# Kernel optimization log

Measured on AMD Instinct MI355X. Metric: run time of the kernel, lower is better.

Reference implementation:

```python
import jax, jax.numpy as jnp
import numpy as np

EPS = 1e-6  # flax nn.LayerNorm default epsilon


def excl_cumsum(a, axis):
    c = jnp.roll(jnp.cumsum(a, axis=axis), 1, axis=axis)
    idx = [slice(None)] * a.ndim
    idx[axis] = slice(0, 1)
    return c.at[tuple(idx)].set(0.0)


def mixed_chunk_attn(q, k, v, n_chunks):
    # Mixed chunk linear attention (https://arxiv.org/pdf/2202.10447.pdf)
    if n_chunks == 1:
        mask = jnp.tri(q.shape[1], q.shape[1], -1, dtype=q.dtype)
        qk = jnp.einsum('bls,bms->blm', q, k) * mask
        return jnp.einsum('blm,bme->ble', qk, v)
    B, L = q.shape[:2]
    C = L // n_chunks
    qc = q.reshape(B, n_chunks, C, -1)
    kc = k.reshape(B, n_chunks, C, -1)
    vc = v.reshape(B, n_chunks, C, -1)
    # global linear attention across chunks (exclusive prefix of kv states)
    kv = excl_cumsum(jnp.einsum('bgcs,bgce->bgse', kc, vc), axis=1)
    glob = jnp.einsum('bgcs,bgse->bgce', qc, kv)
    # local strictly-causal quadratic attention within each chunk
    mask = jnp.tri(C, C, -1, dtype=q.dtype)
    qk = jnp.einsum('bgns,bgms->bgnm', qc, kc) * mask
    loc = jnp.einsum('bgnm,bgme->bgne', qk, vc)
    return (glob + loc).reshape(B, L, -1)


def ln_normalize(x):
    mu = jnp.mean(x, axis=-1, keepdims=True)
    var = jnp.mean(jnp.square(x - mu), axis=-1, keepdims=True)
    return (x - mu) * jax.lax.rsqrt(var + EPS)


def fwblock(x, labels, weights, W1, b1, W2, b2, ln_scale, ln_bias, Wu, bu, step_sizes, n_chunks):
    B, L, D = x.shape
    F = W1.shape[1]

    # slow-weight forward with zero perturbations; grad wrt perturbations gives
    # per-token gradients at each layer's output (rank-one fast-weight updates).
    def slow_loss(p1, p3, p_scale, p_bias):
        h1 = x @ W1 + b1 + p1                    # FWDense(4D) + output perturbation
        h2 = jnp.square(jax.nn.relu(h1))         # FWSquaredRelu (paramless)
        h3 = h2 @ W2 + b2 + p3                   # FWDense(D) + output perturbation
        h4 = ln_normalize(h3) * (ln_scale + p_scale) + (ln_bias + p_bias)
        logits = h4 @ Wu + bu
        ll = -jnp.sum(jax.nn.log_softmax(logits) * labels, axis=-1)
        loss = jnp.sum(weights * ll) / jnp.maximum(jnp.sum(weights), 1e-8)
        return loss, h2

    zeros = (jnp.zeros((B, L, F), x.dtype), jnp.zeros((B, L, D), x.dtype),
             jnp.zeros((B, L, D), x.dtype), jnp.zeros((B, L, D), x.dtype))
    (g1, g3, g_scale, g_bias), h2_slow = jax.grad(
        slow_loss, argnums=(0, 1, 2, 3), has_aux=True)(*zeros)

    # fast-weight forward: rank-one weight updates expressed as causal linear attn
    x1 = x @ W1 + b1 - step_sizes[0] * mixed_chunk_attn(x, x, g1, n_chunks)
    x2 = jnp.square(jax.nn.relu(x1))             # step_sizes[1] unused (no params)
    x3 = x2 @ W2 + b2 - step_sizes[2] * mixed_chunk_attn(x2, h2_slow, g3, n_chunks)
    fast_scale = ln_scale - step_sizes[3] * excl_cumsum(g_scale, axis=1)
    fast_bias = ln_bias - step_sizes[3] * excl_cumsum(g_bias, axis=1)
    x4 = ln_normalize(x3) * fast_scale + fast_bias
    return x4 @ Wu + bu


def setup_inputs():
    key = jax.random.key(0)
    ks = jax.random.split(key, 6)
    B, L, D, V = 2, 2048, 1024, 8192
    F = 4 * D
    x = jax.random.normal(ks[0], (B, L, D), jnp.float32)
    labels = jax.random.uniform(ks[1], (B, L, V), jnp.float32)
    weights = jnp.ones((B, L), jnp.float32)
    W1 = jax.random.normal(ks[2], (D, F), jnp.float32) / np.sqrt(D).astype(np.float32)
    b1 = jnp.zeros((F,), jnp.float32)
    W2 = jax.random.normal(ks[3], (F, D), jnp.float32) / np.sqrt(F).astype(np.float32)
    b2 = jnp.zeros((D,), jnp.float32)
    ln_scale = jnp.ones((D,), jnp.float32)
    ln_bias = jnp.zeros((D,), jnp.float32)
    Wu = jax.random.normal(ks[4], (D, V), jnp.float32) / np.sqrt(D).astype(np.float32)
    bu = jnp.zeros((V,), jnp.float32)
    step_sizes = jnp.full((4,), 0.01, jnp.float32)
    return dict(x=x, labels=labels, weights=weights, W1=W1, b1=b1, W2=W2, b2=b2,
                ln_scale=ln_scale, ln_bias=ln_bias, Wu=Wu, bu=bu,
                step_sizes=step_sizes, n_chunks=16)


def reference(x, labels, weights, W1, b1, W2, b2, ln_scale, ln_bias, Wu, bu, step_sizes, n_chunks):
    return fwblock(x, labels, weights, W1, b1, W2, b2, ln_scale, ln_bias, Wu, bu, step_sizes, n_chunks)
```

## Files before the change

kernel.cpp:

```cpp
#include <hip/hip_runtime.h>
#include <cstdint>

typedef unsigned short ushort_t;
typedef __bf16 bf16x8 __attribute__((ext_vector_type(8)));
typedef float f32x4 __attribute__((ext_vector_type(4)));
typedef ushort_t us8 __attribute__((ext_vector_type(8)));

__device__ __forceinline__ ushort_t f2bf(float f) {
  union { float f; unsigned int u; } v; v.f = f;
  unsigned int u = v.u;
  unsigned int r = (u + 0x7fffu + ((u >> 16) & 1u)) >> 16;
  return (ushort_t)r;
}
__device__ __forceinline__ float bf2f(ushort_t u) {
  union { unsigned int u; float f; } v; v.u = ((unsigned int)u) << 16; return v.f;
}

#define GLOAD16(gp, lp)                                                              \
  __builtin_amdgcn_global_load_lds(                                                  \
      reinterpret_cast<const __attribute__((address_space(1))) unsigned int*>(       \
          reinterpret_cast<uintptr_t>(gp)),                                          \
      reinterpret_cast<__attribute__((address_space(3))) unsigned int*>(             \
          reinterpret_cast<uintptr_t>(lp)),                                          \
      16, 0, 0)

struct GemmP {
  const ushort_t* A; const ushort_t* B;
  int M, N, K;
  long long sA, sB;
  float* outf;   long long sOutF;
  ushort_t* outb; long long sOutB;
  ushort_t* outb2;
  const float* bias;
  const float* auxf; long long sAuxF;
  const ushort_t* auxb;
  const float* steps;
  float* part; int ksplit, Kc, Tt;
};

template <int EPI>
__global__ __launch_bounds__(256) void gemm_bt(GemmP p) {
  const int nwg = gridDim.x * gridDim.y;
  const int orig = blockIdx.y * gridDim.x + blockIdx.x;
  const int xcd = orig & 7, loc = orig >> 3;
  const int q8 = nwg >> 3, r8 = nwg & 7;
  const int wg = (xcd < r8) ? (xcd * (q8 + 1) + loc) : (r8 * (q8 + 1) + (xcd - r8) * q8 + loc);
  int mt, nt;
  if (EPI == 7) {
    int t_ = wg;
    mt = (int)((sqrtf(8.f * t_ + 1.f) - 1.f) * 0.5f);
    while ((mt + 1) * (mt + 2) / 2 <= t_) mt++;
    while (mt * (mt + 1) / 2 > t_) mt--;
    nt = t_ - mt * (mt + 1) / 2;
  } else {
    nt = wg % gridDim.x; mt = wg / gridDim.x;
  }
  const int m0 = mt * 128, n0 = nt * 128;

  int bz = blockIdx.z, ks = 0;
  if (EPI == 6 || EPI == 7) { bz = blockIdx.z / p.ksplit; ks = blockIdx.z % p.ksplit; }

  const ushort_t* A = p.A + (size_t)bz * p.sA;
  const ushort_t* B = p.B + (size_t)bz * p.sB;

  int kbeg = 0, kend = p.K;
  if (EPI == 6 || EPI == 7) { kbeg = ks * p.Kc; kend = kbeg + p.Kc; }
  else if (EPI == 4 || EPI == 5) kend = min(p.K, m0 + 128);

  __shared__ ushort_t sA[2 * 128 * 32];
  __shared__ ushort_t sB[2 * 128 * 32];

  const int tid = threadIdx.x;
  const int wid = tid >> 6, lane = tid & 63;
  const int wm = wid >> 1, wn = wid & 1;

  f32x4 acc[4][4];
#pragma unroll
  for (int i = 0; i < 4; i++)
#pragma unroll
    for (int j = 0; j < 4; j++) acc[i][j] = f32x4{0.f, 0.f, 0.f, 0.f};

  const int lr = lane >> 2;
  const int lcsw = (((lane & 3) ^ ((lr >> 1) & 3)) * 8);
  const int rA0 = wid * 16 + lr;
  const int rA1 = 64 + wid * 16 + lr;
  const ushort_t* gA0 = A + (size_t)(m0 + rA0) * p.K + lcsw;
  const ushort_t* gA1 = A + (size_t)(m0 + rA1) * p.K + lcsw;
  const ushort_t* gB0 = B + (size_t)(n0 + rA0) * p.K + lcsw;
  const ushort_t* gB1 = B + (size_t)(n0 + rA1) * p.K + lcsw;
  ushort_t* lA0 = &sA[wid * 512];
  ushort_t* lA1 = &sA[(4 + wid) * 512];
  ushort_t* lB0 = &sB[wid * 512];
  ushort_t* lB1 = &sB[(4 + wid) * 512];

  const int fr = lane & 15;
  const int q = lane >> 4;
  const int slot = (q ^ ((fr >> 1) & 3)) * 8;
  int offA[4], offB[4];
#pragma unroll
  for (int i = 0; i < 4; i++) offA[i] = (wm * 4 + i) * 512 + fr * 32 + slot;
#pragma unroll
  for (int j = 0; j < 4; j++) offB[j] = (wn * 4 + j) * 512 + fr * 32 + slot;

  const int nT = (kend - kbeg) >> 5;
  auto stage = [&](int t) {
    const int kk = kbeg + t * 32;
    const int o = (t & 1) * 4096;
    GLOAD16(gA0 + kk, lA0 + o);
    GLOAD16(gA1 + kk, lA1 + o);
    GLOAD16(gB0 + kk, lB0 + o);
    GLOAD16(gB1 + kk, lB1 + o);
  };
  stage(0);
  asm volatile("s_waitcnt vmcnt(0)" ::: "memory");
  __builtin_amdgcn_s_barrier();

  for (int t = 0; t < nT; ++t) {
    const int co = (t & 1) * 4096;
    if (t + 1 < nT) stage(t + 1);
    __builtin_amdgcn_sched_barrier(0);
    bf16x8 av[4], bv[4];
#pragma unroll
    for (int j = 0; j < 4; j++) bv[j] = *reinterpret_cast<const bf16x8*>(&sB[co + offB[j]]);
#pragma unroll
    for (int i = 0; i < 4; i++) av[i] = *reinterpret_cast<const bf16x8*>(&sA[co + offA[i]]);
    __builtin_amdgcn_s_setprio(1);
#pragma unroll
    for (int i = 0; i < 4; i++)
#pragma unroll
      for (int j = 0; j < 4; j++)
        acc[i][j] = __builtin_amdgcn_mfma_f32_16x16x32_bf16(av[i], bv[j], acc[i][j], 0, 0, 0);
    __builtin_amdgcn_s_setprio(0);
    asm volatile("s_waitcnt vmcnt(0)" ::: "memory");
    __builtin_amdgcn_s_barrier();
  }

  const int fq = q;
  float ss = 0.f;
  if (EPI == 4) ss = p.steps[0];
  else if (EPI == 5) ss = p.steps[2];
  float* outf = p.outf ? p.outf + (size_t)bz * p.sOutF : nullptr;
  ushort_t* outb = p.outb ? p.outb + (size_t)bz * p.sOutB : nullptr;
  ushort_t* outb2 = p.outb2;
  const float* auxf = p.auxf ? p.auxf + (size_t)bz * p.sAuxF : nullptr;
  const ushort_t* auxb = p.auxb ? p.auxb + (size_t)bz * p.sAuxF : nullptr;
  float* partT = nullptr;
  if (EPI == 6) partT = p.part + (size_t)blockIdx.z * p.M * p.N;
  if (EPI == 7) partT = p.part + ((size_t)blockIdx.z * p.Tt + wg) * 16384;

#pragma unroll
  for (int i = 0; i < 4; i++) {
#pragma unroll
    for (int j = 0; j < 4; j++) {
#pragma unroll
      for (int r2 = 0; r2 < 4; r2++) {
        int lrow = wm * 64 + i * 16 + fq * 4 + r2;
        int lcol = wn * 64 + j * 16 + fr;
        int row = m0 + lrow, col = n0 + lcol;
        size_t g = (size_t)row * p.N + col;
        float v = acc[i][j][r2];
        if (EPI == 0) {
          outf[g] = v + (p.bias ? p.bias[col] : 0.f);
        } else if (EPI == 8) {
          outb[g] = f2bf(v + p.bias[col]);
        } else if (EPI == 1) {
          v += p.bias[col];
          outb[g] = f2bf(v);
          float rl = fmaxf(v, 0.f);
          outb2[g] = f2bf(rl * rl);
        } else if (EPI == 2) {
          outb[g] = f2bf(v * 2.f * sqrtf(bf2f(auxb[g])));
        } else if (EPI == 4) {
          float x1 = bf2f(auxb[g]) - ss * v;
          float rl = fmaxf(x1, 0.f);
          outb[g] = f2bf(rl * rl);
        } else if (EPI == 5) {
          outf[g] = auxf[g] - ss * v;
        } else if (EPI == 6) {
          partT[g] = v;
        } else if (EPI == 7) {
          partT[lrow * 128 + lcol] = v;
        }
      }
    }
  }
}

template <int EPI>
__global__ __launch_bounds__(512, 2) void gemm256(GemmP p) {
  const int nwg = gridDim.x * gridDim.y;
  const int orig = blockIdx.y * gridDim.x + blockIdx.x;
  const int xcd = orig & 7, loc = orig >> 3;
  const int q8 = nwg >> 3, r8 = nwg & 7;
  const int wg = (xcd < r8) ? (xcd * (q8 + 1) + loc) : (r8 * (q8 + 1) + (xcd - r8) * q8 + loc);
  const int nt = wg % gridDim.x, mt = wg / gridDim.x;
  const int m0 = mt * 256, n0 = nt * 256;
  const int bz = blockIdx.z;

  const ushort_t* A = p.A + (size_t)bz * p.sA;
  const ushort_t* B = p.B + (size_t)bz * p.sB;
  const int kend = p.K;

  extern __shared__ ushort_t smem[];
  ushort_t* sA = smem;
  ushort_t* sB = smem + 4 * 8192;

  const int tid = threadIdx.x;
  const int wid = tid >> 6, lane = tid & 63;
  const int wm = wid >> 2, wn = wid & 3;

  f32x4 acc[8][4];
#pragma unroll
  for (int i = 0; i < 8; i++)
#pragma unroll
    for (int j = 0; j < 4; j++) acc[i][j] = f32x4{0.f, 0.f, 0.f, 0.f};

  const int lr = lane >> 2;
  const int lcsw = (((lane & 3) ^ ((lr >> 1) & 3)) * 8);
  const int rT0 = wid * 16 + lr;
  const int rT1 = 128 + wid * 16 + lr;
  const ushort_t* gA0 = A + (size_t)(m0 + rT0) * p.K + lcsw;
  const ushort_t* gA1 = A + (size_t)(m0 + rT1) * p.K + lcsw;
  const ushort_t* gB0 = B + (size_t)(n0 + rT0) * p.K + lcsw;
  const ushort_t* gB1 = B + (size_t)(n0 + rT1) * p.K + lcsw;
  ushort_t* lA0 = &sA[wid * 512];
  ushort_t* lA1 = &sA[(8 + wid) * 512];
  ushort_t* lB0 = &sB[wid * 512];
  ushort_t* lB1 = &sB[(8 + wid) * 512];

  const int fr = lane & 15;
  const int q = lane >> 4;
  const int slot = (q ^ ((fr >> 1) & 3)) * 8;
  int offA[8], offB[4];
#pragma unroll
  for (int i = 0; i < 8; i++) offA[i] = (wm * 8 + i) * 512 + fr * 32 + slot;
#pragma unroll
  for (int j = 0; j < 4; j++) offB[j] = (wn * 4 + j) * 512 + fr * 32 + slot;

  const int nT = kend >> 5;
  auto stage4 = [&](int t) {
    const int kk = t * 32;
    const int o = (t & 3) * 8192;
    GLOAD16(gA0 + kk, lA0 + o);
    GLOAD16(gA1 + kk, lA1 + o);
    GLOAD16(gB0 + kk, lB0 + o);
    GLOAD16(gB1 + kk, lB1 + o);
  };
  stage4(0);
  if (nT > 1) stage4(1);
  if (nT > 2) stage4(2);
  if (nT > 2)      { asm volatile("s_waitcnt vmcnt(8)" ::: "memory"); }
  else if (nT > 1) { asm volatile("s_waitcnt vmcnt(4)" ::: "memory"); }
  else             { asm volatile("s_waitcnt vmcnt(0)" ::: "memory"); }
  __builtin_amdgcn_s_barrier();

  for (int t = 0; t < nT; ++t) {
    const int co = (t & 3) * 8192;
    if (t + 3 < nT) stage4(t + 3);
    __builtin_amdgcn_sched_barrier(0);
    bf16x8 av[8], bv[4];
#pragma unroll
    for (int j = 0; j < 4; j++) bv[j] = *reinterpret_cast<const bf16x8*>(&sB[co + offB[j]]);
#pragma unroll
    for (int i = 0; i < 8; i++) av[i] = *reinterpret_cast<const bf16x8*>(&sA[co + offA[i]]);
    __builtin_amdgcn_s_setprio(1);
#pragma unroll
    for (int i = 0; i < 8; i++)
#pragma unroll
      for (int j = 0; j < 4; j++)
        acc[i][j] = __builtin_amdgcn_mfma_f32_16x16x32_bf16(av[i], bv[j], acc[i][j], 0, 0, 0);
    __builtin_amdgcn_s_setprio(0);
    if (t + 3 < nT)      { asm volatile("s_waitcnt vmcnt(8)" ::: "memory"); }
    else if (t + 2 < nT) { asm volatile("s_waitcnt vmcnt(4)" ::: "memory"); }
    else if (t + 1 < nT) { asm volatile("s_waitcnt vmcnt(0)" ::: "memory"); }
    __builtin_amdgcn_s_barrier();
  }

  const int fq = q;
  float* outf = p.outf;
  ushort_t* outb = p.outb;

#pragma unroll
  for (int i = 0; i < 8; i++) {
#pragma unroll
    for (int j = 0; j < 4; j++) {
#pragma unroll
      for (int r2 = 0; r2 < 4; r2++) {
        int row = m0 + wm * 128 + i * 16 + fq * 4 + r2;
        int col = n0 + wn * 64 + j * 16 + fr;
        size_t g = (size_t)row * p.N + col;
        float v = acc[i][j][r2];
        if (EPI == 0) {
          outf[g] = v + p.bias[col];
        } else if (EPI == 8) {
          outb[g] = f2bf(v + p.bias[col]);
        }
      }
    }
  }
}

__global__ __launch_bounds__(256) void k_comb(const float* part, const float* bias, float* out,
                                              int N, size_t MN, int S) {
  size_t e = ((size_t)blockIdx.x * 256 + threadIdx.x) * 4;
  if (e >= MN) return;
  float4 s = *(const float4*)(part + e);
  for (int p_ = 1; p_ < S; p_++) {
    float4 v = *(const float4*)(part + (size_t)p_ * MN + e);
    s.x += v.x; s.y += v.y; s.z += v.z; s.w += v.w;
  }
  if (bias) {
    int col = (int)(e % (size_t)N);
    s.x += bias[col]; s.y += bias[col + 1]; s.z += bias[col + 2]; s.w += bias[col + 3];
  }
  *(float4*)(out + e) = s;
}

__global__ __launch_bounds__(256) void k_combtri(const float* part, ushort_t* out, int Tt, int S,
                                                 int L) {
  int t = blockIdx.x, bz = blockIdx.y;
  int mt = (int)((sqrtf(8.f * t + 1.f) - 1.f) * 0.5f);
  while ((mt + 1) * (mt + 2) / 2 <= t) mt++;
  while (mt * (mt + 1) / 2 > t) mt--;
  int nt = t - mt * (mt + 1) / 2;
  const float* pb = part + ((size_t)bz * S * Tt + t) * 16384;
  ushort_t* ob = out + (size_t)bz * L * L;
  for (int e4 = threadIdx.x; e4 < 4096; e4 += 256) {
    int e = e4 * 4;
    float4 s = *(const float4*)(pb + e);
    for (int p_ = 1; p_ < S; p_++) {
      float4 v = *(const float4*)(pb + (size_t)p_ * Tt * 16384 + e);
      s.x += v.x; s.y += v.y; s.z += v.z; s.w += v.w;
    }
    int lr = e >> 7, lc2 = e & 127;
    int row = mt * 128 + lr, col = nt * 128 + lc2;
    ushort4 o;
    o.x = (col < row) ? f2bf(s.x) : (ushort_t)0;
    o.y = (col + 1 < row) ? f2bf(s.y) : (ushort_t)0;
    o.z = (col + 2 < row) ? f2bf(s.z) : (ushort_t)0;
    o.w = (col + 3 < row) ? f2bf(s.w) : (ushort_t)0;
    *(ushort4*)(&ob[(size_t)row * L + col]) = o;
  }
}

__global__ __launch_bounds__(256) void k_conv(const float* in, ushort_t* out, size_t n) {
  size_t i = ((size_t)blockIdx.x * 256 + threadIdx.x) * 4;
  if (i >= n) return;
  float4 v = *(const float4*)(in + i);
  out[i] = f2bf(v.x); out[i + 1] = f2bf(v.y); out[i + 2] = f2bf(v.z); out[i + 3] = f2bf(v.w);
}

__global__ __launch_bounds__(256) void k_tconv(const float* in, ushort_t* out, int R, int C) {
  __shared__ float t[32][33];
  int c0 = blockIdx.x * 32, r0 = blockIdx.y * 32;
  int tx = threadIdx.x & 31, ty = threadIdx.x >> 5;
#pragma unroll
  for (int i = ty; i < 32; i += 8) t[i][tx] = in[(size_t)(r0 + i) * C + c0 + tx];
  __syncthreads();
#pragma unroll
  for (int i = ty; i < 32; i += 8) out[(size_t)(c0 + i) * R + r0 + tx] = f2bf(t[tx][i]);
}

__global__ __launch_bounds__(256) void k_wprep(const float* in, ushort_t* outS, ushort_t* outT,
                                               int R, int C) {
  __shared__ float t[32][33];
  int c0 = blockIdx.x * 32, r0 = blockIdx.y * 32;
  int tx = threadIdx.x & 31, ty = threadIdx.x >> 5;
#pragma unroll
  for (int i = ty; i < 32; i += 8) {
    float v = in[(size_t)(r0 + i) * C + c0 + tx];
    t[i][tx] = v;
    outS[(size_t)(r0 + i) * C + c0 + tx] = f2bf(v);
  }
  __syncthreads();
#pragma unroll
  for (int i = ty; i < 32; i += 8) outT[(size_t)(c0 + i) * R + r0 + tx] = f2bf(t[tx][i]);
}

__global__ __launch_bounds__(256) void k_tb2b(const ushort_t* in, ushort_t* out, int L, int C) {
  __shared__ ushort_t t[32][33];
  int b = blockIdx.z;
  const ushort_t* ib = in + (size_t)b * L * C;
  ushort_t* ob = out + (size_t)b * C * L;
  int c0 = blockIdx.x * 32, l0 = blockIdx.y * 32;
  int tx = threadIdx.x & 31, ty = threadIdx.x >> 5;
#pragma unroll
  for (int i = ty; i < 32; i += 8) t[i][tx] = ib[(size_t)(l0 + i) * C + c0 + tx];
  __syncthreads();
#pragma unroll
  for (int i = ty; i < 32; i += 8) ob[(size_t)(c0 + i) * L + l0 + tx] = t[tx][i];
}

__device__ __forceinline__ void blockRed2(float& a, float& b, float* red) {
#pragma unroll
  for (int o = 32; o; o >>= 1) { a += __shfl_down(a, o); b += __shfl_down(b, o); }
  int w = threadIdx.x >> 6;
  if ((threadIdx.x & 63) == 0) { red[w] = a; red[4 + w] = b; }
  __syncthreads();
  a = red[0] + red[1] + red[2] + red[3];
  b = red[4] + red[5] + red[6] + red[7];
  __syncthreads();
}

__global__ __launch_bounds__(256) void k_lncomb(const float* part, const float* bias,
                                                const float* sc, const float* bi, float* nout,
                                                float* rstd, ushort_t* yb, size_t MN, int D,
                                                int S) {
  __shared__ float red[8];
  int row = blockIdx.x;
  int d = threadIdx.x * 4;
  size_t g = (size_t)row * D + d;
  float4 v = *(const float4*)(part + g);
  for (int s_ = 1; s_ < S; s_++) {
    float4 w = *(const float4*)(part + (size_t)s_ * MN + g);
    v.x += w.x; v.y += w.y; v.z += w.z; v.w += w.w;
  }
  float4 bb = *(const float4*)(bias + d);
  v.x += bb.x; v.y += bb.y; v.z += bb.z; v.w += bb.w;
  float s1 = v.x + v.y + v.z + v.w;
  float s2 = v.x * v.x + v.y * v.y + v.z * v.z + v.w * v.w;
  blockRed2(s1, s2, red);
  float mu = s1 / D;
  float var = s2 / D - mu * mu;
  float rs = rsqrtf(var + 1e-6f);
  float4 nv;
  nv.x = (v.x - mu) * rs; nv.y = (v.y - mu) * rs; nv.z = (v.z - mu) * rs; nv.w = (v.w - mu) * rs;
  *(float4*)(nout + g) = nv;
  float4 scv = *(const float4*)(sc + d);
  float4 biv = *(const float4*)(bi + d);
  ushort4 o;
  o.x = f2bf(nv.x * scv.x + biv.x);
  o.y = f2bf(nv.y * scv.y + biv.y);
  o.z = f2bf(nv.z * scv.z + biv.z);
  o.w = f2bf(nv.w * scv.w + biv.w);
  *(ushort4*)(yb + g) = o;
  if (threadIdx.x == 0) rstd[row] = rs;
}

__global__ __launch_bounds__(256) void k_lnfwd2(const float* X, const float* fs, const float* fb,
                                                ushort_t* yb, int D) {
  __shared__ float red[8];
  int row = blockIdx.x;
  const float* x = X + (size_t)row * D;
  float s = 0.f, s2 = 0.f;
  for (int d = threadIdx.x; d < D; d += 256) { float v = x[d]; s += v; s2 += v * v; }
  blockRed2(s, s2, red);
  float mu = s / D;
  float var = s2 / D - mu * mu;
  float rs = rsqrtf(var + 1e-6f);
  for (int d = threadIdx.x; d < D; d += 256) {
    size_t g = (size_t)row * D + d;
    float nv = (x[d] - mu) * rs;
    yb[g] = f2bf(nv * fs[g] + fb[g]);
  }
}

__global__ __launch_bounds__(256) void k_lnbwd(const float* G, const float* nn, const float* rstd,
                                               const float* sc, ushort_t* g3b, float* gsc, int D) {
  __shared__ float red[8];
  int row = blockIdx.x;
  const float* g = G + (size_t)row * D;
  const float* n_ = nn + (size_t)row * D;
  float sa = 0.f, sb = 0.f;
  for (int d = threadIdx.x; d < D; d += 256) {
    float dn = g[d] * sc[d];
    sa += dn; sb += dn * n_[d];
  }
  blockRed2(sa, sb, red);
  float a = sa / D, b = sb / D, rs = rstd[row];
  for (int d = threadIdx.x; d < D; d += 256) {
    size_t gi = (size_t)row * D + d;
    float dn = g[d] * sc[d];
    g3b[gi] = f2bf(rs * (dn - a - n_[d] * b));
    gsc[gi] = g[d] * n_[d];
  }
}

__global__ __launch_bounds__(256) void k_wsum(const float* w, float* o, int n) {
  __shared__ float red[4];
  float s = 0.f;
  for (int i = threadIdx.x; i < n; i += 256) s += w[i];
#pragma unroll
  for (int d = 32; d; d >>= 1) s += __shfl_down(s, d);
  if ((threadIdx.x & 63) == 0) red[threadIdx.x >> 6] = s;
  __syncthreads();
  if (threadIdx.x == 0) o[0] = fmaxf(red[0] + red[1] + red[2] + red[3], 1e-8f);
}

__global__ __launch_bounds__(256) void k_softgrad(const ushort_t* logits, const float* labels,
                                                  const float* w, const float* wsum,
                                                  ushort_t* dlb, int V) {
  __shared__ float red[8];
  const int row = blockIdx.x;
  const int tid = threadIdx.x;
  const ushort_t* l = logits + (size_t)row * V + tid * 32;
  const float* y = labels + (size_t)row * V + tid * 32;
  float lv[32], yv[32];
#pragma unroll
  for (int i = 0; i < 4; i++) {
    us8 u = *reinterpret_cast<const us8*>(l + i * 8);
#pragma unroll
    for (int j = 0; j < 8; j++) lv[i * 8 + j] = bf2f(u[j]);
  }
#pragma unroll
  for (int i = 0; i < 8; i++) {
    float4 v = *reinterpret_cast<const float4*>(y + i * 4);
    yv[i * 4] = v.x; yv[i * 4 + 1] = v.y; yv[i * 4 + 2] = v.z; yv[i * 4 + 3] = v.w;
  }
  float m = lv[0], t = yv[0];
#pragma unroll
  for (int i = 1; i < 32; i++) { m = fmaxf(m, lv[i]); t += yv[i]; }
#pragma unroll
  for (int o = 32; o; o >>= 1) { m = fmaxf(m, __shfl_down(m, o)); t += __shfl_down(t, o); }
  int wv = tid >> 6;
  if ((tid & 63) == 0) { red[wv] = m; red[4 + wv] = t; }
  __syncthreads();
  m = fmaxf(fmaxf(red[0], red[1]), fmaxf(red[2], red[3]));
  t = red[4] + red[5] + red[6] + red[7];
  __syncthreads();
  float s = 0.f;
#pragma unroll
  for (int i = 0; i < 32; i++) { lv[i] = expf(lv[i] - m); s += lv[i]; }
#pragma unroll
  for (int o = 32; o; o >>= 1) s += __shfl_down(s, o);
  if ((tid & 63) == 0) red[wv] = s;
  __syncthreads();
  s = red[0] + red[1] + red[2] + red[3];
  float c = w[row] / wsum[0];
  float ci = c * t / s;
  ushort_t* dl = dlb + (size_t)row * V + tid * 32;
#pragma unroll
  for (int i = 0; i < 4; i++) {
    us8 o;
#pragma unroll
    for (int j = 0; j < 8; j++) o[j] = f2bf(ci * lv[i * 8 + j] - c * yv[i * 8 + j]);
    *reinterpret_cast<us8*>(dl + i * 8) = o;
  }
}

__global__ __launch_bounds__(256) void k_scanpart(const float* gs, const float* gb, float* ps,
                                                  float* pb, int L, int D) {
  int d = blockIdx.x * 256 + threadIdx.x;
  int seg = blockIdx.y, b = blockIdx.z;
  const int SEGL = L / 16;
  size_t base = ((size_t)b * L + seg * SEGL) * D + d;
  float s1 = 0.f, s2 = 0.f;
  for (int i = 0; i < SEGL; i++) { s1 += gs[base + (size_t)i * D]; s2 += gb[base + (size_t)i * D]; }
  size_t pi = ((size_t)b * 16 + seg) * D + d;
  ps[pi] = s1; pb[pi] = s2;
}

__global__ __launch_bounds__(256) void k_scanapply(const float* gs, const float* gb,
                                                   const float* ps, const float* pb,
                                                   const float* sc, const float* bi,
                                                   const float* steps, float* fs, float* fb,
                                                   int L, int D) {
  int d = blockIdx.x * 256 + threadIdx.x;
  int seg = blockIdx.y, b = blockIdx.z;
  const int SEGL = L / 16;
  float ss = steps[3];
  float rs_ = 0.f, rb_ = 0.f;
  for (int s = 0; s < seg; s++) {
    size_t pi = ((size_t)b * 16 + s) * D + d;
    rs_ += ps[pi]; rb_ += pb[pi];
  }
  float s0 = sc[d], b0 = bi[d];
  size_t base = ((size_t)b * L + seg * SEGL) * D + d;
  for (int i = 0; i < SEGL; i++) {
    size_t g = base + (size_t)i * D;
    fs[g] = s0 - ss * rs_;
    fb[g] = b0 - ss * rb_;
    rs_ += gs[g]; rb_ += gb[g];
  }
}

extern "C" void kernel_launch(void* const* d_in, const int* in_sizes, int n_in, void* d_out,
                              int out_size, void* d_ws, size_t ws_size, hipStream_t stream) {
  const float* x        = (const float*)d_in[0];
  const float* labels   = (const float*)d_in[1];
  const float* weights  = (const float*)d_in[2];
  const float* W1       = (const float*)d_in[3];
  const float* b1       = (const float*)d_in[4];
  const float* W2       = (const float*)d_in[5];
  const float* b2       = (const float*)d_in[6];
  const float* ln_scale = (const float*)d_in[7];
  const float* ln_bias  = (const float*)d_in[8];
  const float* Wu       = (const float*)d_in[9];
  const float* bu       = (const float*)d_in[10];
  const float* steps    = (const float*)d_in[11];

  const int BL = in_sizes[2];
  const int D  = in_sizes[7];
  const int F  = in_sizes[4];
  const int V  = in_sizes[10];
  const int Bb = 2, L = BL / Bb;
  const int T1t = (L / 128) * (L / 128 + 1) / 2;
  const unsigned SMEM = 4 * 8192 * 2 * 2;

  char* ws = (char*)d_ws;
  size_t off = 0;
  auto take = [&](size_t b) { char* p = ws + off; off = (off + b + 255) & ~(size_t)255; return p; };

  ushort_t* xb   = (ushort_t*)take((size_t)BL * D * 2);
  ushort_t* w1t  = (ushort_t*)take((size_t)F * D * 2);
  ushort_t* w2t  = (ushort_t*)take((size_t)D * F * 2);
  ushort_t* w2b  = (ushort_t*)take((size_t)F * D * 2);
  ushort_t* wut  = (ushort_t*)take((size_t)V * D * 2);
  ushort_t* wub  = (ushort_t*)take((size_t)D * V * 2);
  ushort_t* H1b  = (ushort_t*)take((size_t)BL * F * 2);
  ushort_t* H2b  = (ushort_t*)take((size_t)BL * F * 2);
  float*    nbuf = (float*)take((size_t)BL * D * 4);
  float*    rstd = (float*)take((size_t)BL * 4);
  ushort_t* h4b  = (ushort_t*)take((size_t)BL * D * 2);
  float*    wsumb= (float*)take(256);
  float*    G4   = (float*)take((size_t)BL * D * 4);
  float*    gsc  = (float*)take((size_t)BL * D * 4);
  ushort_t* g3b  = (ushort_t*)take((size_t)BL * D * 2);
  ushort_t* g3t  = (ushort_t*)take((size_t)BL * D * 2);
  float*    fs   = (float*)take((size_t)BL * D * 4);
  float*    fb   = (float*)take((size_t)BL * D * 4);
  ushort_t* x4b  = (ushort_t*)take((size_t)BL * D * 2);
  float*    psc  = (float*)take((size_t)Bb * 16 * D * 4);
  float*    pbi  = (float*)take((size_t)Bb * 16 * D * 4);
  char* poolA = take((size_t)BL * V * 4);
  ushort_t* logitsb = (ushort_t*)poolA;
  float*    partA  = (float*)poolA;
  ushort_t* g1b = (ushort_t*)poolA;
  ushort_t* g1t = (ushort_t*)(poolA + (size_t)BL * F * 2);
  ushort_t* S1b = (ushort_t*)(poolA + (size_t)BL * F * 4);
  ushort_t* x2b = (ushort_t*)(poolA + (size_t)BL * F * 4 + (size_t)Bb * L * L * 2);
  char* poolB = take((size_t)BL * V * 2);
  ushort_t* dlb = (ushort_t*)poolB;
  float*    partS1 = (float*)poolB;
  ushort_t* S2b = (ushort_t*)poolB;
  float*    X3  = (float*)(poolB + (size_t)Bb * L * L * 2);
  float*    x3  = (float*)(poolB + (size_t)Bb * L * L * 2 + (size_t)BL * D * 4);

  dim3 blk(256), blk5(512);
  const size_t MN_D = (size_t)BL * D;

  k_conv<<<dim3((unsigned)((size_t)BL * D / 1024)), blk, 0, stream>>>(x, xb, (size_t)BL * D);
  k_tconv<<<dim3(F / 32, D / 32), blk, 0, stream>>>(W1, w1t, D, F);
  k_wprep<<<dim3(D / 32, F / 32), blk, 0, stream>>>(W2, w2b, w2t, F, D);
  k_wprep<<<dim3(V / 32, D / 32), blk, 0, stream>>>(Wu, wub, wut, D, V);

  GemmP p;
  auto clr = [&]() { p = GemmP{}; };

  clr(); p.A = xb; p.B = w1t; p.M = BL; p.N = F; p.K = D;
  p.outb = H1b; p.outb2 = H2b; p.bias = b1;
  gemm_bt<1><<<dim3(F / 128, BL / 128, 1), blk, 0, stream>>>(p);
  clr(); p.A = H2b; p.B = w2t; p.M = BL; p.N = D; p.K = F;
  p.part = partA; p.ksplit = 4; p.Kc = F / 4;
  gemm_bt<6><<<dim3(D / 128, BL / 128, 4), blk, 0, stream>>>(p);
  k_lncomb<<<dim3(BL), blk, 0, stream>>>(partA, b2, ln_scale, ln_bias, nbuf, rstd, h4b, MN_D, D, 4);
  clr(); p.A = h4b; p.B = wut; p.M = BL; p.N = V; p.K = D; p.outb = logitsb; p.bias = bu;
  gemm256<8><<<dim3(V / 256, BL / 256, 1), blk5, SMEM, stream>>>(p);
  k_wsum<<<dim3(1), blk, 0, stream>>>(weights, wsumb, BL);
  k_softgrad<<<dim3(BL), blk, 0, stream>>>(logitsb, labels, weights, wsumb, dlb, V);
  clr(); p.A = dlb; p.B = wub; p.M = BL; p.N = D; p.K = V;
  p.part = partA; p.ksplit = 4; p.Kc = V / 4;
  gemm_bt<6><<<dim3(D / 128, BL / 128, 4), blk, 0, stream>>>(p);
  k_comb<<<dim3((unsigned)(MN_D / 1024)), blk, 0, stream>>>(partA, nullptr, G4, D, MN_D, 4);
  k_lnbwd<<<dim3(BL), blk, 0, stream>>>(G4, nbuf, rstd, ln_scale, g3b, gsc, D);
  clr(); p.A = g3b; p.B = w2b; p.M = BL; p.N = F; p.K = D; p.outb = g1b; p.auxb = H2b;
  gemm_bt<2><<<dim3(F / 128, BL / 128, 1), blk, 0, stream>>>(p);
  k_tb2b<<<dim3(F / 32, L / 32, Bb), blk, 0, stream>>>(g1b, g1t, L, F);
  k_tb2b<<<dim3(D / 32, L / 32, Bb), blk, 0, stream>>>(g3b, g3t, L, D);
  clr(); p.A = xb; p.B = xb; p.M = L; p.N = L; p.K = D;
  p.sA = (long long)L * D; p.sB = (long long)L * D;
  p.part = partS1; p.ksplit = 2; p.Kc = D / 2; p.Tt = T1t;
  gemm_bt<7><<<dim3(T1t, 1, Bb * 2), blk, 0, stream>>>(p);
  k_combtri<<<dim3(T1t, Bb), blk, 0, stream>>>(partS1, S1b, T1t, 2, L);
  clr(); p.A = S1b; p.B = g1t; p.M = L; p.N = F; p.K = L;
  p.sA = (long long)L * L; p.sB = (long long)F * L;
  p.outb = x2b; p.sOutB = (long long)L * F; p.auxb = H1b; p.sAuxF = (long long)L * F;
  p.steps = steps;
  gemm_bt<4><<<dim3(F / 128, L / 128, Bb), blk, 0, stream>>>(p);
  clr(); p.A = x2b; p.B = w2t; p.M = BL; p.N = D; p.K = F;
  p.part = partA; p.ksplit = 4; p.Kc = F / 4;
  gemm_bt<6><<<dim3(D / 128, BL / 128, 4), blk, 0, stream>>>(p);
  k_comb<<<dim3((unsigned)(MN_D / 1024)), blk, 0, stream>>>(partA, b2, X3, D, MN_D, 4);
  clr(); p.A = x2b; p.B = H2b; p.M = L; p.N = L; p.K = F;
  p.sA = (long long)L * F; p.sB = (long long)L * F;
  p.part = partA; p.ksplit = 2; p.Kc = F / 2; p.Tt = T1t;
  gemm_bt<7><<<dim3(T1t, 1, Bb * 2), blk, 0, stream>>>(p);
  k_combtri<<<dim3(T1t, Bb), blk, 0, stream>>>(partA, S2b, T1t, 2, L);
  clr(); p.A = S2b; p.B = g3t; p.M = L; p.N = D; p.K = L;
  p.sA = (long long)L * L; p.sB = (long long)D * L;
  p.outf = x3; p.sOutF = (long long)L * D; p.auxf = X3; p.sAuxF = (long long)L * D; p.steps = steps;
  gemm_bt<5><<<dim3(D / 128, L / 128, Bb), blk, 0, stream>>>(p);
  k_scanpart<<<dim3(D / 256, 16, Bb), blk, 0, stream>>>(gsc, G4, psc, pbi, L, D);
  k_scanapply<<<dim3(D / 256, 16, Bb), blk, 0, stream>>>(gsc, G4, psc, pbi, ln_scale, ln_bias,
                                                         steps, fs, fb, L, D);
  k_lnfwd2<<<dim3(BL), blk, 0, stream>>>(x3, fs, fb, x4b, D);
  clr(); p.A = x4b; p.B = wut; p.M = BL; p.N = V; p.K = D; p.outf = (float*)d_out; p.bias = bu;
  gemm256<0><<<dim3(V / 256, BL / 256, 1), blk5, SMEM, stream>>>(p);
}
```

Measured before the change: 1.103 ms.

## Replace direct global-to-LDS loads with register-staged double-buffered GEMM pipeline

Both GEMM kernels stop using global_load_lds and instead load tiles into registers, then write them to LDS one phase later, with two register sets alternating across an unrolled-by-two loop. The 256-tile kernel drops from a 4-stage LDS ring to 2 stages, which halves shared memory, and its min-blocks launch bound is removed. The intent is to hide global latency behind compute using registers rather than LDS depth. In exchange it costs more VGPRs and adds explicit LDS store instructions, and losing the occupancy hint may reduce occupancy. The gemm256 kernel also drops the blockIdx.z batch offset.

```diff
diff --git a/kernel.cpp b/kernel.cpp
--- a/kernel.cpp
+++ b/kernel.cpp
@@ -5,6 +5,7 @@
 typedef __bf16 bf16x8 __attribute__((ext_vector_type(8)));
 typedef float f32x4 __attribute__((ext_vector_type(4)));
 typedef ushort_t us8 __attribute__((ext_vector_type(8)));
+typedef unsigned int u32x4 __attribute__((ext_vector_type(4)));
 
 __device__ __forceinline__ ushort_t f2bf(float f) {
   union { float f; unsigned int u; } v; v.f = f;
@@ -15,14 +16,6 @@
 __device__ __forceinline__ float bf2f(ushort_t u) {
   union { unsigned int u; float f; } v; v.u = ((unsigned int)u) << 16; return v.f;
 }
-
-#define GLOAD16(gp, lp)                                                              \
-  __builtin_amdgcn_global_load_lds(                                                  \
-      reinterpret_cast<const __attribute__((address_space(1))) unsigned int*>(       \
-          reinterpret_cast<uintptr_t>(gp)),                                          \
-      reinterpret_cast<__attribute__((address_space(3))) unsigned int*>(             \
-          reinterpret_cast<uintptr_t>(lp)),                                          \
-      16, 0, 0)
 
 struct GemmP {
   const ushort_t* A; const ushort_t* B;
@@ -37,6 +30,19 @@
   const float* steps;
   float* part; int ksplit, Kc, Tt;
 };
+
+
+#define LOADT_BT(t, S)                                                        \
+  { const int kk_ = kbeg + (t) * 32;                                          \
+    rA0##S = *(const u32x4*)(gA0 + kk_); rA1##S = *(const u32x4*)(gA1 + kk_); \
+    rB0##S = *(const u32x4*)(gB0 + kk_); rB1##S = *(const u32x4*)(gB1 + kk_); }
+#define STORET_BT(o, S)                                                       \
+  { *(u32x4*)(wA0 + (o)) = rA0##S; *(u32x4*)(wA1 + (o)) = rA1##S;             \
+    *(u32x4*)(wB0 + (o)) = rB0##S; *(u32x4*)(wB1 + (o)) = rB1##S; }
+#define PHASE_END()                                                           \
+  { asm volatile("s_waitcnt lgkmcnt(0)" ::: "memory");                        \
+    __builtin_amdgcn_sched_barrier(0);                                        \
+    __builtin_amdgcn_s_barrier(); }
 
 template <int EPI>
 __global__ __launch_bounds__(256) void gemm_bt(GemmP p) {
@@ -82,16 +88,16 @@
 
   const int lr = lane >> 2;
   const int lcsw = (((lane & 3) ^ ((lr >> 1) & 3)) * 8);
-  const int rA0 = wid * 16 + lr;
-  const int rA1 = 64 + wid * 16 + lr;
-  const ushort_t* gA0 = A + (size_t)(m0 + rA0) * p.K + lcsw;
-  const ushort_t* gA1 = A + (size_t)(m0 + rA1) * p.K + lcsw;
-  const ushort_t* gB0 = B + (size_t)(n0 + rA0) * p.K + lcsw;
-  const ushort_t* gB1 = B + (size_t)(n0 + rA1) * p.K + lcsw;
-  ushort_t* lA0 = &sA[wid * 512];
-  ushort_t* lA1 = &sA[(4 + wid) * 512];
-  ushort_t* lB0 = &sB[wid * 512];
-  ushort_t* lB1 = &sB[(4 + wid) * 512];
+  const int rA0r = wid * 16 + lr;
+  const int rA1r = 64 + wid * 16 + lr;
+  const ushort_t* gA0 = A + (size_t)(m0 + rA0r) * p.K + lcsw;
+  const ushort_t* gA1 = A + (size_t)(m0 + rA1r) * p.K + lcsw;
+  const ushort_t* gB0 = B + (size_t)(n0 + rA0r) * p.K + lcsw;
+  const ushort_t* gB1 = B + (size_t)(n0 + rA1r) * p.K + lcsw;
+  ushort_t* wA0 = &sA[wid * 512 + lane * 8];
+  ushort_t* wA1 = &sA[(4 + wid) * 512 + lane * 8];
+  ushort_t* wB0 = &sB[wid * 512 + lane * 8];
+  ushort_t* wB1 = &sB[(4 + wid) * 512 + lane * 8];
 
   const int fr = lane & 15;
   const int q = lane >> 4;
@@ -103,22 +109,10 @@
   for (int j = 0; j < 4; j++) offB[j] = (wn * 4 + j) * 512 + fr * 32 + slot;
 
   const int nT = (kend - kbeg) >> 5;
-  auto stage = [&](int t) {
-    const int kk = kbeg + t * 32;
-    const int o = (t & 1) * 4096;
-    GLOAD16(gA0 + kk, lA0 + o);
-    GLOAD16(gA1 + kk, lA1 + o);
-    GLOAD16(gB0 + kk, lB0 + o);
-    GLOAD16(gB1 + kk, lB1 + o);
-  };
-  stage(0);
-  asm volatile("s_waitcnt vmcnt(0)" ::: "memory");
-  __builtin_amdgcn_s_barrier();
-
-  for (int t = 0; t < nT; ++t) {
-    const int co = (t & 1) * 4096;
-    if (t + 1 < nT) stage(t + 1);
-    __builtin_amdgcn_sched_barrier(0);
+  u32x4 rA0e, rA1e, rB0e, rB1e;
+  u32x4 rA0o, rA1o, rB0o, rB1o;
+
+  auto compute = [&](int co) {
     bf16x8 av[4], bv[4];
 #pragma unroll
     for (int j = 0; j < 4; j++) bv[j] = *reinterpret_cast<const bf16x8*>(&sB[co + offB[j]]);
@@ -131,8 +125,24 @@
       for (int j = 0; j < 4; j++)
         acc[i][j] = __builtin_amdgcn_mfma_f32_16x16x32_bf16(av[i], bv[j], acc[i][j], 0, 0, 0);
     __builtin_amdgcn_s_setprio(0);
-    asm volatile("s_waitcnt vmcnt(0)" ::: "memory");
-    __builtin_amdgcn_s_barrier();
+  };
+
+  LOADT_BT(0, e);
+  STORET_BT(0, e);
+  if (nT > 1) LOADT_BT(1, o);
+  PHASE_END();
+
+  for (int t = 0; t < nT; t += 2) {
+    compute(0);
+    if (t + 1 < nT) STORET_BT(4096, o);
+    if (t + 2 < nT) LOADT_BT(t + 2, e);
+    PHASE_END();
+    if (t + 1 < nT) {
+      compute(4096);
+      if (t + 2 < nT) STORET_BT(0, e);
+      if (t + 3 < nT) LOADT_BT(t + 3, o);
+      PHASE_END();
+    }
   }
 
   const int fq = q;
@@ -187,7 +197,7 @@
 }
 
 template <int EPI>
-__global__ __launch_bounds__(512, 2) void gemm256(GemmP p) {
+__global__ __launch_bounds__(512) void gemm256(GemmP p) {
   const int nwg = gridDim.x * gridDim.y;
   const int orig = blockIdx.y * gridDim.x + blockIdx.x;
   const int xcd = orig & 7, loc = orig >> 3;
@@ -195,15 +205,14 @@
   const int wg = (xcd < r8) ? (xcd * (q8 + 1) + loc) : (r8 * (q8 + 1) + (xcd - r8) * q8 + loc);
   const int nt = wg % gridDim.x, mt = wg / gridDim.x;
   const int m0 = mt * 256, n0 = nt * 256;
-  const int bz = blockIdx.z;
-
-  const ushort_t* A = p.A + (size_t)bz * p.sA;
-  const ushort_t* B = p.B + (size_t)bz * p.sB;
-  const int kend = p.K;
+
+  const ushort_t* A = p.A;
+  const ushort_t* B = p.B;
+  const int kbeg = 0, kend = p.K;
 
   extern __shared__ ushort_t smem[];
   ushort_t* sA = smem;
-  ushort_t* sB = smem + 4 * 8192;
+  ushort_t* sB = smem + 2 * 8192;
 
   const int tid = threadIdx.x;
   const int wid = tid >> 6, lane = tid & 63;
@@ -223,10 +232,10 @@
   const ushort_t* gA1 = A + (size_t)(m0 + rT1) * p.K + lcsw;
   const ushort_t* gB0 = B + (size_t)(n0 + rT0) * p.K + lcsw;
   const ushort_t* gB1 = B + (size_t)(n0 + rT1) * p.K + lcsw;
-  ushort_t* lA0 = &sA[wid * 512];
-  ushort_t* lA1 = &sA[(8 + wid) * 512];
-  ushort_t* lB0 = &sB[wid * 512];
-  ushort_t* lB1 = &sB[(8 + wid) * 512];
+  ushort_t* wA0 = &sA[wid * 512 + lane * 8];
+  ushort_t* wA1 = &sA[(8 + wid) * 512 + lane * 8];
+  ushort_t* wB0 = &sB[wid * 512 + lane * 8];
+  ushort_t* wB1 = &sB[(8 + wid) * 512 + lane * 8];
 
   const int fr = lane & 15;
   const int q = lane >> 4;
@@ -237,27 +246,11 @@
 #pragma unroll
   for (int j = 0; j < 4; j++) offB[j] = (wn * 4 + j) * 512 + fr * 32 + slot;
 
-  const int nT = kend >> 5;
-  auto stage4 = [&](int t) {
-    const int kk = t * 32;
-    const int o = (t & 3) * 8192;
-    GLOAD16(gA0 + kk, lA0 + o);
-    GLOAD16(gA1 + kk, lA1 + o);
-    GLOAD16(gB0 + kk, lB0 + o);
-    GLOAD16(gB1 + kk, lB1 + o);
-  };
-  stage4(0);
-  if (nT > 1) stage4(1);
-  if (nT > 2) stage4(2);
-  if (nT > 2)      { asm volatile("s_waitcnt vmcnt(8)" ::: "memory"); }
-  else if (nT > 1) { asm volatile("s_waitcnt vmcnt(4)" ::: "memory"); }
-  else             { asm volatile("s_waitcnt vmcnt(0)" ::: "memory"); }
-  __builtin_amdgcn_s_barrier();
-
-  for (int t = 0; t < nT; ++t) {
-    const int co = (t & 3) * 8192;
-    if (t + 3 < nT) stage4(t + 3);
-    __builtin_amdgcn_sched_barrier(0);
+  const int nT = (kend - kbeg) >> 5;
+  u32x4 rA0e, rA1e, rB0e, rB1e;
+  u32x4 rA0o, rA1o, rB0o, rB1o;
+
+  auto compute = [&](int co) {
     bf16x8 av[8], bv[4];
 #pragma unroll
     for (int j = 0; j < 4; j++) bv[j] = *reinterpret_cast<const bf16x8*>(&sB[co + offB[j]]);
@@ -270,10 +263,24 @@
       for (int j = 0; j < 4; j++)
         acc[i][j] = __builtin_amdgcn_mfma_f32_16x16x32_bf16(av[i], bv[j], acc[i][j], 0, 0, 0);
     __builtin_amdgcn_s_setprio(0);
-    if (t + 3 < nT)      { asm volatile("s_waitcnt vmcnt(8)" ::: "memory"); }
-    else if (t + 2 < nT) { asm volatile("s_waitcnt vmcnt(4)" ::: "memory"); }
-    else if (t + 1 < nT) { asm volatile("s_waitcnt vmcnt(0)" ::: "memory"); }
-    __builtin_amdgcn_s_barrier();
+  };
+
+  LOADT_BT(0, e);
+  STORET_BT(0, e);
+  if (nT > 1) LOADT_BT(1, o);
+  PHASE_END();
+
+  for (int t = 0; t < nT; t += 2) {
+    compute(0);
+    if (t + 1 < nT) STORET_BT(8192, o);
+    if (t + 2 < nT) LOADT_BT(t + 2, e);
+    PHASE_END();
+    if (t + 1 < nT) {
+      compute(8192);
+      if (t + 2 < nT) STORET_BT(0, e);
+      if (t + 3 < nT) LOADT_BT(t + 3, o);
+      PHASE_END();
+    }
   }
 
   const int fq = q;
@@ -595,7 +602,7 @@
   const int V  = in_sizes[10];
   const int Bb = 2, L = BL / Bb;
   const int T1t = (L / 128) * (L / 128 + 1) / 2;
-  const unsigned SMEM = 4 * 8192 * 2 * 2;
+  const unsigned SMEM = 2 * 16384 * 2;
 
   char* ws = (char*)d_ws;
   size_t off = 0;
```

Measured after the change: 1.108 ms. Within noise of the previous version (+0.5%).
